# Kernel optimization log

Measured on AMD Instinct MI355X. Metric: run time of the kernel, lower is better.

The kernel has to match this reference:

```python
import math
import jax, jax.numpy as jnp
import numpy as np
from jax import lax

B, S, D = 2, 1024, 768
H, E, DH = 12, 8, 64          # n_head, num_experts, head dim
KA = 1                        # top-k experts per head (attention)
KF = 2                        # top-k experts per token (FFN)
DFF = 2048
EMA_DECAY = 0.99
CAP_FACTOR = 1.25
NEG_INF = -1e9


def setup_inputs() -> dict:
    key = jax.random.key(0)
    ks = jax.random.split(key, 16)
    sc = 0.02
    x = jax.random.normal(ks[0], (B, S, D), jnp.float32)
    causal = jnp.tril(jnp.ones((S, S), jnp.float32))
    mask = jnp.where(causal > 0, 0.0, NEG_INF).astype(jnp.float32)
    return {
        "x": x,
        "mask": mask,
        "W_q": jax.random.normal(ks[1], (D, D), jnp.float32) * sc,
        "W_k": jax.random.normal(ks[2], (D, D), jnp.float32) * sc,
        "W_v": jax.random.normal(ks[3], (H, E, DH, DH), jnp.float32) * sc,
        "W_o": jax.random.normal(ks[4], (H, E, DH, DH), jnp.float32) * sc,
        "W_router": jax.random.normal(ks[5], (D, H * E), jnp.float32) * sc,
        "g1": jnp.ones((D,), jnp.float32),
        "b1": jnp.zeros((D,), jnp.float32),
        "g2": jnp.ones((D,), jnp.float32),
        "b2": jnp.zeros((D,), jnp.float32),
        "gate_ff": jax.random.normal(ks[6], (D, E), jnp.float32) * sc,
        "W1": jax.random.normal(ks[7], (E, D, DFF), jnp.float32) * sc,
        "W2": jax.random.normal(ks[8], (E, DFF, D), jnp.float32) * sc,
    }


def layer_norm(x, g, b, eps=1e-5):
    m = jnp.mean(x, -1, keepdims=True)
    v = jnp.var(x, -1, keepdims=True)
    return (x - m) * lax.rsqrt(v + eps) * g + b


def head_switch_attention(x, mask, W_q, W_k, W_v, W_o, W_router):
    b, s, d = x.shape
    q = (x @ W_q).reshape(b, s, H, DH)
    k = (x @ W_k).reshape(b, s, H, DH)
    scores = jnp.einsum("bshd,bthd->bhst", q, k) / math.sqrt(DH) + mask
    p_attn = jax.nn.softmax(scores, axis=-1)          # (B,H,S,S)
    gate_logits = (x @ W_router).reshape(b, s, H, E)
    topk_scores, topk_idx = lax.top_k(gate_logits, KA)  # (B,S,H,KA)
    probs = jax.nn.softmax(topk_scores, axis=-1)
    x_h = x.reshape(b, s, H, DH)
    # value projections for all experts (small d_h x d_h GEMMs)
    v_all = jnp.einsum("bshd,hedf->bshef", x_h, W_v)
    y = jnp.zeros_like(x_h)
    hard_counts = jnp.zeros((H, E), jnp.float32)
    for slot in range(KA):
        oh = jax.nn.one_hot(topk_idx[..., slot], E, dtype=x.dtype)  # (B,S,H,E)
        v_sel = jnp.einsum("bshef,bshe->bshf", v_all, oh)
        # faithful to original einsum 'bhst,hbsd->hbtd' (sums over s)
        attn_out = jnp.einsum("bhst,bshf->bthf", p_attn, v_sel)
        o_all = jnp.einsum("bthf,hefg->btheg", attn_out, W_o)
        o_sel = jnp.einsum("btheg,bthe->bthg", o_all, oh)
        y = y + o_sel * probs[..., slot][..., None]
        hard_counts = hard_counts + lax.stop_gradient(oh).sum((0, 1))
    y = y.reshape(b, s, d)
    # EMA buffers start at zero -> ema = (1-decay)*hard/denom
    ema = hard_counts / (b * s * KA) * (1.0 - EMA_DECAY)
    p_lb = ema / (ema.sum() + 1e-9)
    aux = (p_lb * p_lb).sum() * E * H
    return y, aux


def moe_ffn(x, gate_ff, W1, W2):
    b, s, d = x.shape
    gate_logits = x @ gate_ff                      # (B,S,E), eval: no noise
    topk_scores, topk_idx = lax.top_k(gate_logits, KF)
    probs = jax.nn.softmax(topk_scores, axis=-1)   # (B,S,KF)
    capacity = math.ceil(CAP_FACTOR * (b * s) / E)
    flat_idx = topk_idx.reshape(-1)                # (B*S*KF,)
    oh_flat = jax.nn.one_hot(flat_idx, E, dtype=jnp.float32)
    tokens_so_far = jnp.cumsum(oh_flat, axis=0)
    keep = jnp.take_along_axis(tokens_so_far <= capacity, flat_idx[:, None], axis=1)[:, 0]
    probs = probs * keep.reshape(b, s, KF).astype(probs.dtype)
    probs = probs / (probs.sum(-1, keepdims=True) + 1e-9)
    oh = jax.nn.one_hot(topk_idx, E, dtype=probs.dtype)   # (B,S,KF,E)
    w = (probs[..., None] * oh).sum(2).reshape(b * s, E)  # combined weight per (token, expert)
    xf = x.reshape(b * s, d)
    yf = jnp.zeros_like(xf)
    for e in range(E):
        # scaling applied BEFORE ReLU, matching original x_sel = x * weight
        xe = xf * w[:, e:e + 1]
        yf = yf + jnp.maximum(xe @ W1[e], 0.0) @ W2[e]
    token_ctr = ((probs > 0)[..., None].astype(jnp.float32) * oh).sum((0, 1, 2))
    imp_ctr = (probs[..., None] * oh).sum((0, 1, 2))
    aux = ((token_ctr / token_ctr.sum()) * (imp_ctr / imp_ctr.sum())).sum() * E
    return yf.reshape(b, s, d), aux


def reference(x, mask, W_q, W_k, W_v, W_o, W_router, g1, b1, g2, b2, gate_ff, W1, W2):
    # pre-norm transformer block: x + Attn(LN(x)); x + MoEFFN(LN(x))
    a, aux1 = head_switch_attention(layer_norm(x, g1, b1), mask, W_q, W_k, W_v, W_o, W_router)
    x1 = x + a  # dropout is identity in eval
    f, aux2 = moe_ffn(layer_norm(x1, g2, b2), gate_ff, W1, W2)
    return x1 + f, aux1 + aux2
```

## Files before the change

kernel.cpp:

```cpp
#include <hip/hip_runtime.h>
#include <hip/hip_bf16.h>
#include <cstdint>

typedef __hip_bfloat16 bf16;
typedef __attribute__((ext_vector_type(8))) __bf16 bfrag;
typedef __attribute__((ext_vector_type(4))) float f32x4;

#define B_    2
#define S_    1024
#define D_    768
#define H_    12
#define E_    8
#define DH_   64
#define DFF_  2048
#define CAP_  320
#define CAPP_ 384
#define NTOK  (B_*S_)
#define NTH   (NTOK*H_)
#define QKLD  1536

__device__ __forceinline__ void stage16(const bf16* g, bf16* ldsLane){
#if __has_builtin(__builtin_amdgcn_global_load_lds)
  __builtin_amdgcn_global_load_lds((const __attribute__((address_space(1))) unsigned int*)g,
                                   (__attribute__((address_space(3))) unsigned int*)ldsLane, 16, 0, 0);
#else
  *(bfrag*)ldsLane = *(const bfrag*)g;
#endif
}

__global__ __launch_bounds__(256)
void transp_cvt(const float* __restrict__ src, bf16* __restrict__ dst,
                int K, int N, long sSrc, long sDst, int dstRowOff)
{
  src += (long)blockIdx.z*sSrc;
  dst += (long)blockIdx.z*sDst;
  __shared__ float t[32][33];
  int n0 = blockIdx.x*32, k0 = blockIdx.y*32;
  int tx = threadIdx.x & 31, ty = threadIdx.x >> 5;
#pragma unroll
  for (int r=0;r<4;r++){
    int kk = k0 + ty + r*8, nn = n0 + tx;
    t[ty+r*8][tx] = (nn < N) ? src[(long)kk*N + nn] : 0.f;
  }
  __syncthreads();
#pragma unroll
  for (int r=0;r<4;r++){
    int nn = n0 + ty + r*8;
    if (nn < N) dst[(long)(dstRowOff + nn)*K + k0 + tx] = __float2bfloat16(t[tx][ty+r*8]);
  }
}

__global__ __launch_bounds__(256)
void transp_f32(const float* __restrict__ src, float* __restrict__ dst, int K, int N)
{
  __shared__ float t[32][33];
  int n0 = blockIdx.x*32, k0 = blockIdx.y*32;
  int tx = threadIdx.x & 31, ty = threadIdx.x >> 5;
#pragma unroll
  for (int r=0;r<4;r++){
    int kk = k0 + ty + r*8, nn = n0 + tx;
    t[ty+r*8][tx] = (nn < N) ? src[(long)kk*N + nn] : 0.f;
  }
  __syncthreads();
#pragma unroll
  for (int r=0;r<4;r++){
    int nn = n0 + ty + r*8;
    if (nn < N) dst[(long)nn*K + k0 + tx] = t[tx][ty+r*8];
  }
}

__global__ __launch_bounds__(256)
void gemm_bn64(const bf16* __restrict__ A, const bf16* __restrict__ Bt, void* __restrict__ C,
               int M, int N, int K, long sA, long sB, long sC, int relu, int outBf)
{
  A  += (long)blockIdx.z*sA;
  Bt += (long)blockIdx.z*sB;
  int m0 = blockIdx.y*128, n0 = blockIdx.x*64;
  __shared__ bf16 As[128*32];
  __shared__ bf16 Bs[64*32];
  int tid = threadIdx.x;
  int w = tid >> 6, lane = tid & 63;
  int quad = lane >> 4, l16 = lane & 15;
  int wm = w*32;
  f32x4 acc[2][4] = {};
  int srow = (lane >> 2);
  int scol = (lane & 3)*8;
  const bf16* aBase = A + (long)m0*K;
  const bf16* bBase = Bt + (long)n0*K;
  for (int k0=0; k0<K; k0+=32){
#pragma unroll
    for (int j=0;j<2;j++){
      int c = w*2 + j;
      int row = c*16 + srow;
      stage16(aBase + (long)row*K + k0 + scol, As + c*512 + lane*8);
    }
    {
      int row = w*16 + srow;
      stage16(bBase + (long)row*K + k0 + scol, Bs + w*512 + lane*8);
    }
    __syncthreads();
    bfrag af[2], bfv[4];
#pragma unroll
    for (int t=0;t<2;t++) af[t]  = *(const bfrag*)(As + (wm + t*16 + l16)*32 + quad*8);
#pragma unroll
    for (int t=0;t<4;t++) bfv[t] = *(const bfrag*)(Bs + (t*16 + l16)*32 + quad*8);
#pragma unroll
    for (int ti=0;ti<2;ti++)
#pragma unroll
      for (int tj=0;tj<4;tj++)
        acc[ti][tj] = __builtin_amdgcn_mfma_f32_16x16x32_bf16(af[ti], bfv[tj], acc[ti][tj], 0, 0, 0);
    __syncthreads();
  }
  long zoff = (long)blockIdx.z*sC;
  if (outBf){
    bf16* Cb = (bf16*)C + zoff;
#pragma unroll
    for (int ti=0;ti<2;ti++)
#pragma unroll
      for (int tj=0;tj<4;tj++)
#pragma unroll
        for (int r=0;r<4;r++){
          int row = m0 + wm + ti*16 + quad*4 + r;
          int col = n0 + tj*16 + l16;
          float v = acc[ti][tj][r];
          if (relu) v = fmaxf(v, 0.f);
          Cb[(long)row*N + col] = __float2bfloat16(v);
        }
  } else {
    float* Cf = (float*)C + zoff;
#pragma unroll
    for (int ti=0;ti<2;ti++)
#pragma unroll
      for (int tj=0;tj<4;tj++)
#pragma unroll
        for (int r=0;r<4;r++){
          int row = m0 + wm + ti*16 + quad*4 + r;
          int col = n0 + tj*16 + l16;
          float v = acc[ti][tj][r];
          if (relu) v = fmaxf(v, 0.f);
          Cf[(long)row*N + col] = v;
        }
  }
}

__global__ __launch_bounds__(256)
void ln_kernel(const float* __restrict__ src, const float* __restrict__ g, const float* __restrict__ bb,
               float* __restrict__ dstF, bf16* __restrict__ dstB,
               const float* __restrict__ gateW, float* __restrict__ glog2)
{
  int row = blockIdx.x, tid = threadIdx.x;
  __shared__ float red[256];
  __shared__ float gsum[4][E_];
  float v[3];
#pragma unroll
  for (int j=0;j<3;j++) v[j] = src[(long)row*D_ + tid + j*256];
  float s = v[0]+v[1]+v[2];
  red[tid]=s; __syncthreads();
  for (int o=128;o>0;o>>=1){ if(tid<o) red[tid]+=red[tid+o]; __syncthreads(); }
  float mean = red[0]*(1.0f/D_);
  __syncthreads();
  float sq = 0.f;
#pragma unroll
  for (int j=0;j<3;j++){ float d=v[j]-mean; sq += d*d; }
  red[tid]=sq; __syncthreads();
  for (int o=128;o>0;o>>=1){ if(tid<o) red[tid]+=red[tid+o]; __syncthreads(); }
  float rstd = rsqrtf(red[0]*(1.0f/D_) + 1e-5f);
  float ov[3];
#pragma unroll
  for (int j=0;j<3;j++){
    int d = tid + j*256;
    float o = (v[j]-mean)*rstd*g[d] + bb[d];
    ov[j] = o;
    dstF[(long)row*D_+d] = o;
    if (dstB) dstB[(long)row*D_+d] = __float2bfloat16(o);
  }
  if (gateW){
    float gp[E_] = {};
#pragma unroll
    for (int j=0;j<3;j++){
      int d = tid + j*256;
      const float* gw = gateW + (long)d*E_;
#pragma unroll
      for (int e=0;e<E_;e++) gp[e] += ov[j]*gw[e];
    }
#pragma unroll
    for (int off=1; off<64; off<<=1)
#pragma unroll
      for (int e=0;e<E_;e++) gp[e] += __shfl_xor(gp[e], off);
    if ((tid & 63) == 0)
#pragma unroll
      for (int e=0;e<E_;e++) gsum[tid>>6][e] = gp[e];
    __syncthreads();
    if (tid < E_)
      glog2[(long)row*E_ + tid] = gsum[0][tid]+gsum[1][tid]+gsum[2][tid]+gsum[3][tid];
  }
}

#define RTOK 4
__global__ __launch_bounds__(768)
void router_argmax(const float* __restrict__ ln1, const float* __restrict__ WrT, int* __restrict__ eidx)
{
  int tok0 = blockIdx.x*RTOK;
  int tid = threadIdx.x;
  int col = tid >> 3, seg = tid & 7;
  __shared__ float xrow[RTOK][D_];
  __shared__ float logits[RTOK][96];
  for (int i=tid; i<RTOK*D_; i+=768){
    int t = i >> 9, dpos = i & 767;
    t = i / D_; dpos = i - t*D_;
    xrow[t][dpos] = ln1[(long)(tok0+t)*D_ + dpos];
  }
  __syncthreads();
  const float4* wp = (const float4*)(WrT + (long)col*D_ + seg*96);
  float acc[RTOK] = {};
#pragma unroll
  for (int j=0;j<24;j++){
    float4 w = wp[j];
    int dbase = seg*96 + j*4;
#pragma unroll
    for (int t=0;t<RTOK;t++){
      const float* xr = &xrow[t][dbase];
      acc[t] += xr[0]*w.x + xr[1]*w.y + xr[2]*w.z + xr[3]*w.w;
    }
  }
#pragma unroll
  for (int off=1; off<8; off<<=1)
#pragma unroll
    for (int t=0;t<RTOK;t++) acc[t] += __shfl_xor(acc[t], off);
  if (seg == 0)
#pragma unroll
    for (int t=0;t<RTOK;t++) logits[t][col] = acc[t];
  __syncthreads();
  if (tid < RTOK*H_){
    int t = tid / H_, h = tid % H_;
    const float* p = &logits[t][h*8];
    float best = p[0]; int bi = 0;
#pragma unroll
    for (int e=1;e<8;e++){ float v=p[e]; if (v > best){ best=v; bi=e; } }
    eidx[(tok0+t)*H_ + h] = bi;
  }
}

__global__ __launch_bounds__(64)
void vsel_kernel(const float* __restrict__ ln1, const float* __restrict__ Wv,
                 const int* __restrict__ eidx, bf16* __restrict__ vT)
{
  int blk = blockIdx.x;
  int h = blk % H_, tok = blk / H_;
  int b = tok >> 10, s = tok & 1023;
  int f = threadIdx.x;
  __shared__ float xs[DH_];
  xs[f] = ln1[(long)tok*D_ + h*DH_ + f];
  __syncthreads();
  int e = eidx[blk];
  const float* W = Wv + (long)(h*E_+e)*DH_*DH_;
  float acc = 0.f;
#pragma unroll 8
  for (int d=0; d<DH_; d++) acc += xs[d]*W[d*DH_ + f];
  vT[((long)(b*H_+h)*DH_ + f)*S_ + s] = __float2bfloat16(acc);
}

__global__ __launch_bounds__(256)
void attn_stats_mfma(const bf16* __restrict__ qkB, float* __restrict__ gM, float* __restrict__ gL)
{
  int s0 = blockIdx.x*64;
  int h = blockIdx.y, b = blockIdx.z;
  int tid = threadIdx.x;
  int w = tid >> 6, lane = tid & 63;
  int quad = lane >> 4, l16 = lane & 15;
  __shared__ bf16 ldsQ[64*64];
  __shared__ bf16 ldsK[64*64];
  const bf16* qbase = qkB + ((long)(b*S_ + s0))*QKLD + h*DH_;
#pragma unroll
  for (int j=0;j<2;j++){
    int c = j*256 + tid;
    int row = c >> 3, col8 = (c & 7)*8;
    stage16(qbase + (long)row*QKLD + col8, ldsQ + (j*256 + w*64)*8 + lane*8);
  }
  float m_run[4] = {-1e30f,-1e30f,-1e30f,-1e30f};
  float l_run[4] = {0.f,0.f,0.f,0.f};
  const bf16* kbase = qkB + ((long)(b*S_))*QKLD + 768 + h*DH_;
  int ttEnd = s0 >> 6;
  for (int tt=0; tt<=ttEnd; tt++){
    __syncthreads();
#pragma unroll
    for (int j=0;j<2;j++){
      int c = j*256 + tid;
      int row = c >> 3, col8 = (c & 7)*8;
      stage16(kbase + (long)(tt*64 + row)*QKLD + col8, ldsK + (j*256 + w*64)*8 + lane*8);
    }
    __syncthreads();
    bfrag af0 = *(const bfrag*)(ldsQ + (w*16 + l16)*64 + quad*8);
    bfrag af1 = *(const bfrag*)(ldsQ + (w*16 + l16)*64 + 32 + quad*8);
    f32x4 cfr[4];
#pragma unroll
    for (int j=0;j<4;j++){
      bfrag b0 = *(const bfrag*)(ldsK + (j*16 + l16)*64 + quad*8);
      bfrag b1 = *(const bfrag*)(ldsK + (j*16 + l16)*64 + 32 + quad*8);
      f32x4 z = {};
      z = __builtin_amdgcn_mfma_f32_16x16x32_bf16(af0, b0, z, 0,0,0);
      z = __builtin_amdgcn_mfma_f32_16x16x32_bf16(af1, b1, z, 0,0,0);
      cfr[j] = z;
    }
#pragma unroll
    for (int r=0;r<4;r++){
      int s_g = s0 + w*16 + quad*4 + r;
      float v[4];
#pragma unroll
      for (int j=0;j<4;j++){
        int t_g = tt*64 + j*16 + l16;
        v[j] = (t_g <= s_g) ? cfr[j][r]*0.125f : -1e30f;
      }
      float mt = fmaxf(fmaxf(v[0],v[1]), fmaxf(v[2],v[3]));
#pragma unroll
      for (int mm=1; mm<16; mm<<=1) mt = fmaxf(mt, __shfl_xor(mt, mm));
      float mn = fmaxf(m_run[r], mt);
      float sum = __expf(v[0]-mn)+__expf(v[1]-mn)+__expf(v[2]-mn)+__expf(v[3]-mn);
#pragma unroll
      for (int mm=1; mm<16; mm<<=1) sum += __shfl_xor(sum, mm);
      l_run[r] = l_run[r]*__expf(m_run[r]-mn) + sum;
      m_run[r] = mn;
    }
  }
  if (l16 == 0){
    long base = ((long)(b*H_ + h))*S_ + s0 + w*16 + quad*4;
#pragma unroll
    for (int r=0;r<4;r++){ gM[base+r] = m_run[r]; gL[base+r] = l_run[r]; }
  }
}

__global__ __launch_bounds__(256)
void attn_pv(const bf16* __restrict__ qkB, const bf16* __restrict__ vT,
             const float* __restrict__ gM, const float* __restrict__ gL, float* __restrict__ aoH)
{
  int t0 = blockIdx.x*64;
  int h = blockIdx.y, b = blockIdx.z;
  int bh = b*H_ + h;
  int tid = threadIdx.x;
  int w = tid >> 6, lane = tid & 63;
  int quad = lane >> 4, l16 = lane & 15;
  __shared__ bf16 ldsK[64*64];
  __shared__ bf16 ldsQ[64*64];
  __shared__ bf16 ldsV[64*64];
  __shared__ bf16 ldsS[64*64];
  __shared__ float smx[64], sli[64];
  const bf16* kbase = qkB + ((long)(b*S_ + t0))*QKLD + 768 + h*DH_;
#pragma unroll
  for (int j=0;j<2;j++){
    int c = j*256 + tid;
    int row = c >> 3, col8 = (c & 7)*8;
    stage16(kbase + (long)row*QKLD + col8, ldsK + (j*256 + w*64)*8 + lane*8);
  }
  f32x4 accO[4] = {};
  const bf16* qbase = qkB + ((long)(b*S_))*QKLD + h*DH_;
  const bf16* vbase = vT + ((long)bh*DH_)*S_;
  for (int sb = t0>>6; sb < S_/64; sb++){
    __syncthreads();
#pragma unroll
    for (int j=0;j<2;j++){
      int c = j*256 + tid;
      int row = c >> 3, col8 = (c & 7)*8;
      stage16(qbase + (long)(sb*64 + row)*QKLD + col8, ldsQ + (j*256 + w*64)*8 + lane*8);
      stage16(vbase + (long)row*S_ + sb*64 + col8, ldsV + (j*256 + w*64)*8 + lane*8);
    }
    if (tid < 64){
      smx[tid] = gM[(long)bh*S_ + sb*64 + tid];
      sli[tid] = 1.0f / gL[(long)bh*S_ + sb*64 + tid];
    }
    __syncthreads();
    bfrag af0 = *(const bfrag*)(ldsK + (w*16 + l16)*64 + quad*8);
    bfrag af1 = *(const bfrag*)(ldsK + (w*16 + l16)*64 + 32 + quad*8);
    f32x4 cs[4];
#pragma unroll
    for (int j=0;j<4;j++){
      bfrag b0 = *(const bfrag*)(ldsQ + (j*16 + l16)*64 + quad*8);
      bfrag b1 = *(const bfrag*)(ldsQ + (j*16 + l16)*64 + 32 + quad*8);
      f32x4 z = {};
      z = __builtin_amdgcn_mfma_f32_16x16x32_bf16(af0, b0, z, 0,0,0);
      z = __builtin_amdgcn_mfma_f32_16x16x32_bf16(af1, b1, z, 0,0,0);
      cs[j] = z;
    }
#pragma unroll
    for (int j=0;j<4;j++)
#pragma unroll
      for (int r=0;r<4;r++){
        int t_loc = w*16 + quad*4 + r;
        int s_loc = j*16 + l16;
        float wgt = ((t0 + t_loc) <= (sb*64 + s_loc))
                  ? __expf(cs[j][r]*0.125f - smx[s_loc])*sli[s_loc] : 0.f;
        ldsS[t_loc*64 + s_loc] = __float2bfloat16(wgt);
      }
    bfrag pa0 = *(const bfrag*)(ldsS + (w*16 + l16)*64 + quad*8);
    bfrag pa1 = *(const bfrag*)(ldsS + (w*16 + l16)*64 + 32 + quad*8);
#pragma unroll
    for (int j=0;j<4;j++){
      bfrag b0 = *(const bfrag*)(ldsV + (j*16 + l16)*64 + quad*8);
      bfrag b1 = *(const bfrag*)(ldsV + (j*16 + l16)*64 + 32 + quad*8);
      accO[j] = __builtin_amdgcn_mfma_f32_16x16x32_bf16(pa0, b0, accO[j], 0,0,0);
      accO[j] = __builtin_amdgcn_mfma_f32_16x16x32_bf16(pa1, b1, accO[j], 0,0,0);
    }
  }
#pragma unroll
  for (int j=0;j<4;j++)
#pragma unroll
    for (int r=0;r<4;r++){
      int t_loc = w*16 + quad*4 + r;
      int f = j*16 + l16;
      aoH[((long)bh*S_ + t0 + t_loc)*DH_ + f] = accO[j][r];
    }
}

__global__ __launch_bounds__(64)
void oproj_kernel(const float* __restrict__ aoH, const float* __restrict__ Wo,
                  const int* __restrict__ eidx, const float* __restrict__ x,
                  float* __restrict__ x1)
{
  int blk = blockIdx.x;
  int h = blk % H_, tok = blk / H_;
  int b = tok >> 10, s = tok & 1023;
  int g = threadIdx.x;
  __shared__ float xs[DH_];
  xs[g] = aoH[((long)(b*H_+h)*S_ + s)*DH_ + g];
  __syncthreads();
  int e = eidx[blk];
  const float* W = Wo + (long)(h*E_+e)*DH_*DH_;
  float acc = 0.f;
#pragma unroll 8
  for (int f=0; f<DH_; f++) acc += xs[f]*W[f*DH_ + g];
  long idx = (long)tok*D_ + h*DH_ + g;
  x1[idx] = x[idx] + acc;
}

__global__ __launch_bounds__(256)
void route_kernel(const float* __restrict__ glog2, const int* __restrict__ eidx,
                  int* __restrict__ gI0, int* __restrict__ gI1,
                  int* __restrict__ gPos0, int* __restrict__ gPos1,
                  int* __restrict__ listTok, float* __restrict__ listW,
                  int* __restrict__ gCnt, float* __restrict__ auxOut)
{
  __shared__ unsigned char sI0[NTOK], sI1[NTOK];
  __shared__ float sP0[NTOK], sP1[NTOK];
  __shared__ short sPos0[NTOK], sPos1[NTOK];
  __shared__ int   sScan[256*E_];
  __shared__ int   sHist[H_*E_];
  __shared__ float sImp[E_];
  __shared__ int   sCnt[E_];
  int tid = threadIdx.x;
  if (tid < E_) sImp[tid] = 0.f;
  for (int i=tid; i<NTOK; i+=256){
    const float* p = glog2 + (long)i*E_;
    float b0 = p[0]; int e0 = 0;
#pragma unroll
    for (int e=1;e<E_;e++){ float vv=p[e]; if (vv > b0){ b0=vv; e0=e; } }
    float b1v = -1e30f; int e1 = 0;
#pragma unroll
    for (int e=0;e<E_;e++){ if (e==e0) continue; float vv=p[e]; if (vv > b1v){ b1v=vv; e1=e; } }
    float ex = __expf(b1v - b0);
    float inv = 1.f/(1.f + ex);
    sI0[i] = (unsigned char)e0; sI1[i] = (unsigned char)e1;
    sP0[i] = inv; sP1[i] = ex*inv;
    gI0[i] = e0; gI1[i] = e1;
  }
  __syncthreads();
  {
    int myCnt[E_] = {};
#pragma unroll
    for (int j=0;j<16;j++){
      int i = tid*16 + j;
      int tok = i >> 1;
      int e = (i & 1) ? (int)sI1[tok] : (int)sI0[tok];
      myCnt[e]++;
    }
#pragma unroll
    for (int e=0;e<E_;e++) sScan[tid*E_+e] = myCnt[e];
    __syncthreads();
    for (int off=1; off<256; off<<=1){
      int v[E_];
      if (tid >= off){
#pragma unroll
        for (int e=0;e<E_;e++) v[e] = sScan[(tid-off)*E_+e];
      }
      __syncthreads();
      if (tid >= off){
#pragma unroll
        for (int e=0;e<E_;e++) sScan[tid*E_+e] += v[e];
      }
      __syncthreads();
    }
    int pref[E_];
#pragma unroll
    for (int e=0;e<E_;e++) pref[e] = tid ? sScan[(tid-1)*E_+e] : 0;
#pragma unroll
    for (int j=0;j<16;j++){
      int i = tid*16 + j;
      int tok = i >> 1;
      int e = (i & 1) ? (int)sI1[tok] : (int)sI0[tok];
      int pos = pref[e]++;
      short p = (pos < CAP_) ? (short)pos : (short)-1;
      if (i & 1) sPos1[tok] = p; else sPos0[tok] = p;
    }
    if (tid < E_){
      int cnt = sScan[255*E_ + tid];
      sCnt[tid] = cnt < CAP_ ? cnt : CAP_;
      gCnt[tid] = sCnt[tid];
    }
  }
  __syncthreads();
  for (int i=tid; i<NTOK; i+=256){
    int e0 = sI0[i], e1 = sI1[i];
    int p0i = sPos0[i], p1i = sPos1[i];
    float k0 = p0i >= 0 ? 1.f : 0.f, k1 = p1i >= 0 ? 1.f : 0.f;
    float p0 = sP0[i], p1 = sP1[i];
    float denom = p0*k0 + p1*k1 + 1e-9f;
    float w0 = p0*k0/denom, w1 = p1*k1/denom;
    if (p0i >= 0){ listTok[e0*CAP_+p0i] = i; listW[e0*CAP_+p0i] = w0; atomicAdd(&sImp[e0], w0); }
    if (p1i >= 0){ listTok[e1*CAP_+p1i] = i; listW[e1*CAP_+p1i] = w1; atomicAdd(&sImp[e1], w1); }
    gPos0[i] = p0i; gPos1[i] = p1i;
  }
  if (tid < H_*E_) sHist[tid] = 0;
  __syncthreads();
  for (int j=tid; j<NTH; j+=256){
    int h = j % H_;
    atomicAdd(&sHist[h*E_ + eidx[j]], 1);
  }
  __syncthreads();
  if (tid == 0){
    float tot = 0.f;
    for (int i=0;i<H_*E_;i++) tot += (float)sHist[i]*(1.0f/NTOK)*0.01f;
    float a1 = 0.f;
    for (int i=0;i<H_*E_;i++){
      float p = ((float)sHist[i]*(1.0f/NTOK)*0.01f)/(tot + 1e-9f);
      a1 += p*p;
    }
    a1 *= (float)(H_*E_);
    float tcs = 0.f, ims = 0.f;
    for (int e=0;e<E_;e++){ tcs += (float)sCnt[e]; ims += sImp[e]; }
    float a2 = 0.f;
    for (int e=0;e<E_;e++) a2 += ((float)sCnt[e]/tcs)*(sImp[e]/ims);
    a2 *= (float)E_;
    auxOut[0] = a1 + a2;
  }
}

__global__ __launch_bounds__(256)
void gather_kernel(const float* __restrict__ ln2, const int* __restrict__ listTok,
                   const float* __restrict__ listW, const int* __restrict__ gCnt,
                   bf16* __restrict__ Xg)
{
  int blk = blockIdx.x;
  int e = blk / CAPP_, r = blk % CAPP_;
  int tid = threadIdx.x;
  bool live = r < gCnt[e];
  int tok = 0; float w = 0.f;
  if (live){ tok = listTok[e*CAP_+r]; w = listW[e*CAP_+r]; }
  for (int d=tid; d<D_; d+=256)
    Xg[(long)blk*D_ + d] = __float2bfloat16(live ? ln2[(long)tok*D_+d]*w : 0.f);
}

__global__ __launch_bounds__(256)
void combine_kernel(const float* __restrict__ x1, const float* __restrict__ Yexp,
                    const int* __restrict__ gI0, const int* __restrict__ gI1,
                    const int* __restrict__ gPos0, const int* __restrict__ gPos1,
                    float* __restrict__ out)
{
  int i = blockIdx.x;
  int tid = threadIdx.x;
  int p0 = gPos0[i], p1 = gPos1[i];
  int e0 = gI0[i],  e1 = gI1[i];
  const float* y0 = Yexp + (long)(e0*CAPP_ + (p0 >= 0 ? p0 : 0))*D_;
  const float* y1 = Yexp + (long)(e1*CAPP_ + (p1 >= 0 ? p1 : 0))*D_;
  for (int d=tid; d<D_; d+=256){
    float v = x1[(long)i*D_+d];
    if (p0 >= 0) v += y0[d];
    if (p1 >= 0) v += y1[d];
    out[(long)i*D_+d] = v;
  }
}

extern "C" void kernel_launch(void* const* d_in, const int* in_sizes, int n_in,
                              void* d_out, int out_size, void* d_ws, size_t ws_size,
                              hipStream_t stream)
{
  const float* x    = (const float*)d_in[0];
  const float* W_q  = (const float*)d_in[2];
  const float* W_k  = (const float*)d_in[3];
  const float* W_v  = (const float*)d_in[4];
  const float* W_o  = (const float*)d_in[5];
  const float* W_r  = (const float*)d_in[6];
  const float* g1   = (const float*)d_in[7];
  const float* b1   = (const float*)d_in[8];
  const float* g2   = (const float*)d_in[9];
  const float* b2   = (const float*)d_in[10];
  const float* gate = (const float*)d_in[11];
  const float* W1   = (const float*)d_in[12];
  const float* W2   = (const float*)d_in[13];
  float* out = (float*)d_out;

  float* wsf = (float*)d_ws;
  const long oX1   = 0;
  const long oLnF  = 1572864;
  const long oLnB  = 3145728;
  const long oWcat = 3932160;
  const long oWrT  = 4521984;
  const long oGM   = 4718592;
  const long oGL   = 4743168;
  const long oEidx = 4767744;
  const long oGlg2 = 4792320;
  const long oI0   = 4808704;
  const long oI1   = 4810752;
  const long oP0   = 4812800;
  const long oP1   = 4814848;
  const long oLT   = 4816896;
  const long oLW   = 4819456;
  const long oCnt  = 4822016;
  const long SB    = 4822528;
  const long TOTAL = SB + 12976128;
  if (ws_size < (size_t)TOTAL*4) return;

  float* x1    = wsf + oX1;
  float* lnbF  = wsf + oLnF;
  bf16*  lnbB  = (bf16*)(wsf + oLnB);
  bf16*  WcatB = (bf16*)(wsf + oWcat);
  float* WrT   = wsf + oWrT;
  float* gM    = wsf + oGM;
  float* gL    = wsf + oGL;
  int*   eidx  = (int*)(wsf + oEidx);
  float* glog2 = wsf + oGlg2;
  int*   gI0   = (int*)(wsf + oI0);
  int*   gI1   = (int*)(wsf + oI1);
  int*   gPos0 = (int*)(wsf + oP0);
  int*   gPos1 = (int*)(wsf + oP1);
  int*   lTok  = (int*)(wsf + oLT);
  float* lW    = wsf + oLW;
  int*   gCnt  = (int*)(wsf + oCnt);
  bf16*  qkB   = (bf16*)(wsf + SB);
  bf16*  vT    = (bf16*)(wsf + SB + 1572864);
  float* aoH   = wsf + SB + 2359296;
  bf16*  WT    = (bf16*)(wsf + SB);
  bf16*  Xg    = (bf16*)(wsf + SB + 6291456);
  bf16*  Hid   = (bf16*)(wsf + SB + 7471104);
  float* Yexp  = wsf + SB + 10616832;

  transp_cvt<<<dim3(24,24,1),256,0,stream>>>(W_q, WcatB, 768, 768, 0, 0, 0);
  transp_cvt<<<dim3(24,24,1),256,0,stream>>>(W_k, WcatB, 768, 768, 0, 0, 768);
  transp_f32<<<dim3(3,24,1),256,0,stream>>>(W_r, WrT, 768, 96);

  ln_kernel<<<NTOK,256,0,stream>>>(x, g1, b1, lnbF, lnbB, nullptr, nullptr);
  gemm_bn64<<<dim3(24,16,1),256,0,stream>>>(lnbB, WcatB, qkB, 2048, QKLD, 768, 0,0,0, 0, 1);
  router_argmax<<<NTOK/RTOK,768,0,stream>>>(lnbF, WrT, eidx);
  vsel_kernel<<<NTH,64,0,stream>>>(lnbF, W_v, eidx, vT);
  attn_stats_mfma<<<dim3(S_/64,H_,B_),256,0,stream>>>(qkB, gM, gL);
  attn_pv<<<dim3(S_/64,H_,B_),256,0,stream>>>(qkB, vT, gM, gL, aoH);
  oproj_kernel<<<NTH,64,0,stream>>>(aoH, W_o, eidx, x, x1);

  ln_kernel<<<NTOK,256,0,stream>>>(x1, g2, b2, lnbF, nullptr, gate, glog2);
  route_kernel<<<1,256,0,stream>>>(glog2, eidx, gI0,gI1,gPos0,gPos1, lTok,lW,gCnt, out + (size_t)NTOK*D_);
  gather_kernel<<<E_*CAPP_,256,0,stream>>>(lnbF, lTok, lW, gCnt, Xg);
  transp_cvt<<<dim3(64,24,8),256,0,stream>>>(W1, WT, 768, 2048, (long)768*2048, (long)2048*768, 0);
  gemm_bn64<<<dim3(32,3,8),256,0,stream>>>(Xg, WT, Hid, CAPP_, DFF_, 768,
                                           (long)CAPP_*768, (long)2048*768, (long)CAPP_*2048, 1, 1);
  transp_cvt<<<dim3(24,64,8),256,0,stream>>>(W2, WT, 2048, 768, (long)2048*768, (long)768*2048, 0);
  gemm_bn64<<<dim3(12,3,8),256,0,stream>>>(Hid, WT, Yexp, CAPP_, 768, 2048,
                                           (long)CAPP_*2048, (long)768*2048, (long)CAPP_*768, 0, 0);
  combine_kernel<<<NTOK,256,0,stream>>>(x1, Yexp, gI0,gI1,gPos0,gPos1, out);
}
```

Before: 447.1 us.

## Swizzle LDS layouts in GEMM/attention and move head histogram to router

```diff
diff --git a/kernel.cpp b/kernel.cpp
--- a/kernel.cpp
+++ b/kernel.cpp
@@ -84,26 +84,27 @@
   int wm = w*32;
   f32x4 acc[2][4] = {};
   int srow = (lane >> 2);
-  int scol = (lane & 3)*8;
+  int gsw  = ((lane & 3) ^ (srow & 3))*8;
   const bf16* aBase = A + (long)m0*K;
   const bf16* bBase = Bt + (long)n0*K;
+  int xr = (l16 & 3);
   for (int k0=0; k0<K; k0+=32){
 #pragma unroll
     for (int j=0;j<2;j++){
       int c = w*2 + j;
       int row = c*16 + srow;
-      stage16(aBase + (long)row*K + k0 + scol, As + c*512 + lane*8);
+      stage16(aBase + (long)row*K + k0 + gsw, As + c*512 + lane*8);
     }
     {
       int row = w*16 + srow;
-      stage16(bBase + (long)row*K + k0 + scol, Bs + w*512 + lane*8);
+      stage16(bBase + (long)row*K + k0 + gsw, Bs + w*512 + lane*8);
     }
     __syncthreads();
     bfrag af[2], bfv[4];
 #pragma unroll
-    for (int t=0;t<2;t++) af[t]  = *(const bfrag*)(As + (wm + t*16 + l16)*32 + quad*8);
-#pragma unroll
-    for (int t=0;t<4;t++) bfv[t] = *(const bfrag*)(Bs + (t*16 + l16)*32 + quad*8);
+    for (int t=0;t<2;t++) af[t]  = *(const bfrag*)(As + (wm + t*16 + l16)*32 + ((quad ^ xr)*8));
+#pragma unroll
+    for (int t=0;t<4;t++) bfv[t] = *(const bfrag*)(Bs + (t*16 + l16)*32 + ((quad ^ xr)*8));
 #pragma unroll
     for (int ti=0;ti<2;ti++)
 #pragma unroll
@@ -198,7 +199,8 @@
 
 #define RTOK 4
 __global__ __launch_bounds__(768)
-void router_argmax(const float* __restrict__ ln1, const float* __restrict__ WrT, int* __restrict__ eidx)
+void router_argmax(const float* __restrict__ ln1, const float* __restrict__ WrT,
+                   int* __restrict__ eidx, int* __restrict__ gHist)
 {
   int tok0 = blockIdx.x*RTOK;
   int tid = threadIdx.x;
@@ -206,8 +208,7 @@
   __shared__ float xrow[RTOK][D_];
   __shared__ float logits[RTOK][96];
   for (int i=tid; i<RTOK*D_; i+=768){
-    int t = i >> 9, dpos = i & 767;
-    t = i / D_; dpos = i - t*D_;
+    int t = i / D_, dpos = i - t*D_;
     xrow[t][dpos] = ln1[(long)(tok0+t)*D_ + dpos];
   }
   __syncthreads();
@@ -238,6 +239,7 @@
 #pragma unroll
     for (int e=1;e<8;e++){ float v=p[e]; if (v > best){ best=v; bi=e; } }
     eidx[(tok0+t)*H_ + h] = bi;
+    atomicAdd(&gHist[h*E_ + bi], 1);
   }
 }
 
@@ -268,14 +270,16 @@
   int tid = threadIdx.x;
   int w = tid >> 6, lane = tid & 63;
   int quad = lane >> 4, l16 = lane & 15;
+  int x7 = l16 & 7;
   __shared__ bf16 ldsQ[64*64];
   __shared__ bf16 ldsK[64*64];
   const bf16* qbase = qkB + ((long)(b*S_ + s0))*QKLD + h*DH_;
 #pragma unroll
   for (int j=0;j<2;j++){
     int c = j*256 + tid;
-    int row = c >> 3, col8 = (c & 7)*8;
-    stage16(qbase + (long)row*QKLD + col8, ldsQ + (j*256 + w*64)*8 + lane*8);
+    int row = c >> 3;
+    int gs = ((c & 7) ^ (row & 7))*8;
+    stage16(qbase + (long)row*QKLD + gs, ldsQ + c*8);
   }
   float m_run[4] = {-1e30f,-1e30f,-1e30f,-1e30f};
   float l_run[4] = {0.f,0.f,0.f,0.f};
@@ -286,17 +290,18 @@
 #pragma unroll
     for (int j=0;j<2;j++){
       int c = j*256 + tid;
-      int row = c >> 3, col8 = (c & 7)*8;
-      stage16(kbase + (long)(tt*64 + row)*QKLD + col8, ldsK + (j*256 + w*64)*8 + lane*8);
-    }
-    __syncthreads();
-    bfrag af0 = *(const bfrag*)(ldsQ + (w*16 + l16)*64 + quad*8);
-    bfrag af1 = *(const bfrag*)(ldsQ + (w*16 + l16)*64 + 32 + quad*8);
+      int row = c >> 3;
+      int gs = ((c & 7) ^ (row & 7))*8;
+      stage16(kbase + (long)(tt*64 + row)*QKLD + gs, ldsK + c*8);
+    }
+    __syncthreads();
+    bfrag af0 = *(const bfrag*)(ldsQ + (w*16 + l16)*64 + ((quad     ^ x7)*8));
+    bfrag af1 = *(const bfrag*)(ldsQ + (w*16 + l16)*64 + (((quad+4) ^ x7)*8));
     f32x4 cfr[4];
 #pragma unroll
     for (int j=0;j<4;j++){
-      bfrag b0 = *(const bfrag*)(ldsK + (j*16 + l16)*64 + quad*8);
-      bfrag b1 = *(const bfrag*)(ldsK + (j*16 + l16)*64 + 32 + quad*8);
+      bfrag b0 = *(const bfrag*)(ldsK + (j*16 + l16)*64 + ((quad     ^ x7)*8));
+      bfrag b1 = *(const bfrag*)(ldsK + (j*16 + l16)*64 + (((quad+4) ^ x7)*8));
       f32x4 z = {};
       z = __builtin_amdgcn_mfma_f32_16x16x32_bf16(af0, b0, z, 0,0,0);
       z = __builtin_amdgcn_mfma_f32_16x16x32_bf16(af1, b1, z, 0,0,0);
@@ -339,17 +344,19 @@
   int tid = threadIdx.x;
   int w = tid >> 6, lane = tid & 63;
   int quad = lane >> 4, l16 = lane & 15;
+  int x7 = l16 & 7;
   __shared__ bf16 ldsK[64*64];
   __shared__ bf16 ldsQ[64*64];
   __shared__ bf16 ldsV[64*64];
-  __shared__ bf16 ldsS[64*64];
+  __shared__ bf16 ldsS[64*72];
   __shared__ float smx[64], sli[64];
   const bf16* kbase = qkB + ((long)(b*S_ + t0))*QKLD + 768 + h*DH_;
 #pragma unroll
   for (int j=0;j<2;j++){
     int c = j*256 + tid;
-    int row = c >> 3, col8 = (c & 7)*8;
-    stage16(kbase + (long)row*QKLD + col8, ldsK + (j*256 + w*64)*8 + lane*8);
+    int row = c >> 3;
+    int gs = ((c & 7) ^ (row & 7))*8;
+    stage16(kbase + (long)row*QKLD + gs, ldsK + c*8);
   }
   f32x4 accO[4] = {};
   const bf16* qbase = qkB + ((long)(b*S_))*QKLD + h*DH_;
@@ -359,22 +366,23 @@
 #pragma unroll
     for (int j=0;j<2;j++){
       int c = j*256 + tid;
-      int row = c >> 3, col8 = (c & 7)*8;
-      stage16(qbase + (long)(sb*64 + row)*QKLD + col8, ldsQ + (j*256 + w*64)*8 + lane*8);
-      stage16(vbase + (long)row*S_ + sb*64 + col8, ldsV + (j*256 + w*64)*8 + lane*8);
+      int row = c >> 3;
+      int gs = ((c & 7) ^ (row & 7))*8;
+      stage16(qbase + (long)(sb*64 + row)*QKLD + gs, ldsQ + c*8);
+      stage16(vbase + (long)row*S_ + sb*64 + gs, ldsV + c*8);
     }
     if (tid < 64){
       smx[tid] = gM[(long)bh*S_ + sb*64 + tid];
       sli[tid] = 1.0f / gL[(long)bh*S_ + sb*64 + tid];
     }
     __syncthreads();
-    bfrag af0 = *(const bfrag*)(ldsK + (w*16 + l16)*64 + quad*8);
-    bfrag af1 = *(const bfrag*)(ldsK + (w*16 + l16)*64 + 32 + quad*8);
+    bfrag af0 = *(const bfrag*)(ldsK + (w*16 + l16)*64 + ((quad     ^ x7)*8));
+    bfrag af1 = *(const bfrag*)(ldsK + (w*16 + l16)*64 + (((quad+4) ^ x7)*8));
     f32x4 cs[4];
 #pragma unroll
     for (int j=0;j<4;j++){
-      bfrag b0 = *(const bfrag*)(ldsQ + (j*16 + l16)*64 + quad*8);
-      bfrag b1 = *(const bfrag*)(ldsQ + (j*16 + l16)*64 + 32 + quad*8);
+      bfrag b0 = *(const bfrag*)(ldsQ + (j*16 + l16)*64 + ((quad     ^ x7)*8));
+      bfrag b1 = *(const bfrag*)(ldsQ + (j*16 + l16)*64 + (((quad+4) ^ x7)*8));
       f32x4 z = {};
       z = __builtin_amdgcn_mfma_f32_16x16x32_bf16(af0, b0, z, 0,0,0);
       z = __builtin_amdgcn_mfma_f32_16x16x32_bf16(af1, b1, z, 0,0,0);
@@ -388,14 +396,14 @@
         int s_loc = j*16 + l16;
         float wgt = ((t0 + t_loc) <= (sb*64 + s_loc))
                   ? __expf(cs[j][r]*0.125f - smx[s_loc])*sli[s_loc] : 0.f;
-        ldsS[t_loc*64 + s_loc] = __float2bfloat16(wgt);
+        ldsS[t_loc*72 + s_loc] = __float2bfloat16(wgt);
       }
-    bfrag pa0 = *(const bfrag*)(ldsS + (w*16 + l16)*64 + quad*8);
-    bfrag pa1 = *(const bfrag*)(ldsS + (w*16 + l16)*64 + 32 + quad*8);
+    bfrag pa0 = *(const bfrag*)(ldsS + (w*16 + l16)*72 + quad*8);
+    bfrag pa1 = *(const bfrag*)(ldsS + (w*16 + l16)*72 + 32 + quad*8);
 #pragma unroll
     for (int j=0;j<4;j++){
-      bfrag b0 = *(const bfrag*)(ldsV + (j*16 + l16)*64 + quad*8);
-      bfrag b1 = *(const bfrag*)(ldsV + (j*16 + l16)*64 + 32 + quad*8);
+      bfrag b0 = *(const bfrag*)(ldsV + (j*16 + l16)*64 + ((quad     ^ x7)*8));
+      bfrag b1 = *(const bfrag*)(ldsV + (j*16 + l16)*64 + (((quad+4) ^ x7)*8));
       accO[j] = __builtin_amdgcn_mfma_f32_16x16x32_bf16(pa0, b0, accO[j], 0,0,0);
       accO[j] = __builtin_amdgcn_mfma_f32_16x16x32_bf16(pa1, b1, accO[j], 0,0,0);
     }
@@ -432,7 +440,7 @@
 }
 
 __global__ __launch_bounds__(256)
-void route_kernel(const float* __restrict__ glog2, const int* __restrict__ eidx,
+void route_kernel(const float* __restrict__ glog2, const int* __restrict__ gHist,
                   int* __restrict__ gI0, int* __restrict__ gI1,
                   int* __restrict__ gPos0, int* __restrict__ gPos1,
                   int* __restrict__ listTok, float* __restrict__ listW,
@@ -447,6 +455,7 @@
   __shared__ int   sCnt[E_];
   int tid = threadIdx.x;
   if (tid < E_) sImp[tid] = 0.f;
+  if (tid < H_*E_) sHist[tid] = gHist[tid];
   for (int i=tid; i<NTOK; i+=256){
     const float* p = glog2 + (long)i*E_;
     float b0 = p[0]; int e0 = 0;
@@ -516,12 +525,6 @@
     if (p0i >= 0){ listTok[e0*CAP_+p0i] = i; listW[e0*CAP_+p0i] = w0; atomicAdd(&sImp[e0], w0); }
     if (p1i >= 0){ listTok[e1*CAP_+p1i] = i; listW[e1*CAP_+p1i] = w1; atomicAdd(&sImp[e1], w1); }
     gPos0[i] = p0i; gPos1[i] = p1i;
-  }
-  if (tid < H_*E_) sHist[tid] = 0;
-  __syncthreads();
-  for (int j=tid; j<NTH; j+=256){
-    int h = j % H_;
-    atomicAdd(&sHist[h*E_ + eidx[j]], 1);
   }
   __syncthreads();
   if (tid == 0){
@@ -602,6 +605,7 @@
   const long oLnB  = 3145728;
   const long oWcat = 3932160;
   const long oWrT  = 4521984;
+  const long oHist = 4595712;
   const long oGM   = 4718592;
   const long oGL   = 4743168;
   const long oEidx = 4767744;
@@ -622,6 +626,7 @@
   bf16*  lnbB  = (bf16*)(wsf + oLnB);
   bf16*  WcatB = (bf16*)(wsf + oWcat);
   float* WrT   = wsf + oWrT;
+  int*   gHist = (int*)(wsf + oHist);
   float* gM    = wsf + oGM;
   float* gL    = wsf + oGL;
   int*   eidx  = (int*)(wsf + oEidx);
@@ -641,20 +646,21 @@
   bf16*  Hid   = (bf16*)(wsf + SB + 7471104);
   float* Yexp  = wsf + SB + 10616832;
 
+  hipMemsetAsync(gHist, 0, H_*E_*sizeof(int), stream);
   transp_cvt<<<dim3(24,24,1),256,0,stream>>>(W_q, WcatB, 768, 768, 0, 0, 0);
   transp_cvt<<<dim3(24,24,1),256,0,stream>>>(W_k, WcatB, 768, 768, 0, 0, 768);
   transp_f32<<<dim3(3,24,1),256,0,stream>>>(W_r, WrT, 768, 96);
 
   ln_kernel<<<NTOK,256,0,stream>>>(x, g1, b1, lnbF, lnbB, nullptr, nullptr);
   gemm_bn64<<<dim3(24,16,1),256,0,stream>>>(lnbB, WcatB, qkB, 2048, QKLD, 768, 0,0,0, 0, 1);
-  router_argmax<<<NTOK/RTOK,768,0,stream>>>(lnbF, WrT, eidx);
+  router_argmax<<<NTOK/RTOK,768,0,stream>>>(lnbF, WrT, eidx, gHist);
   vsel_kernel<<<NTH,64,0,stream>>>(lnbF, W_v, eidx, vT);
   attn_stats_mfma<<<dim3(S_/64,H_,B_),256,0,stream>>>(qkB, gM, gL);
   attn_pv<<<dim3(S_/64,H_,B_),256,0,stream>>>(qkB, vT, gM, gL, aoH);
   oproj_kernel<<<NTH,64,0,stream>>>(aoH, W_o, eidx, x, x1);
 
   ln_kernel<<<NTOK,256,0,stream>>>(x1, g2, b2, lnbF, nullptr, gate, glog2);
-  route_kernel<<<1,256,0,stream>>>(glog2, eidx, gI0,gI1,gPos0,gPos1, lTok,lW,gCnt, out + (size_t)NTOK*D_);
+  route_kernel<<<1,256,0,stream>>>(glog2, gHist, gI0,gI1,gPos0,gPos1, lTok,lW,gCnt, out + (size_t)NTOK*D_);
   gather_kernel<<<E_*CAPP_,256,0,stream>>>(lnbF, lTok, lW, gCnt, Xg);
   transp_cvt<<<dim3(64,24,8),256,0,stream>>>(W1, WT, 768, 2048, (long)768*2048, (long)2048*768, 0);
   gemm_bn64<<<dim3(32,3,8),256,0,stream>>>(Xg, WT, Hid, CAPP_, DFF_, 768,
```

Result: no change. 448.6 us (+0.3%).
